# Kernel optimization log

Measured on AMD Instinct MI355X. Metric: run time of the kernel, lower is better.

Reference implementation:

```python
import jax, jax.numpy as jnp
import numpy as np

B, T, C, H = 2, 2048, 1024, 16
HD = C // H  # head dim = 64


def setup_inputs() -> dict:
    key = jax.random.key(0)
    k0, k1, k2 = jax.random.split(key, 3)
    x = jax.random.normal(k0, (B, T, C), jnp.float32)
    W_attn = jax.random.normal(k1, (C, 3 * C), jnp.float32) * 0.02
    b_attn = jnp.zeros((3 * C,), jnp.float32)
    W_proj = jax.random.normal(k2, (C, C), jnp.float32) * 0.02
    b_proj = jnp.zeros((C,), jnp.float32)
    # rope: (1,1,T,HD//2,2,2) stack of 2x2 rotation matrices [[cos,-sin],[sin,cos]]
    inv_freq = 1.0 / (10000.0 ** (jnp.arange(0, HD, 2, dtype=jnp.float32) / HD))
    ang = jnp.arange(T, dtype=jnp.float32)[:, None] * inv_freq[None, :]  # (T, HD//2)
    cos, sin = jnp.cos(ang), jnp.sin(ang)
    rope = jnp.stack([jnp.stack([cos, -sin], -1), jnp.stack([sin, cos], -1)], -2)
    rope = rope[None, None]  # (1,1,T,HD//2,2,2)
    return dict(x=x, W_attn=W_attn, b_attn=b_attn, W_proj=W_proj, b_proj=b_proj, rope=rope)


def reference(x, W_attn, b_attn, W_proj, b_proj, rope):
    Bv, Tv, Cv = x.shape
    Hd = Cv // H
    qkv = x @ W_attn + b_attn                      # (B,T,3C) fused QKV proj
    q, k, v = jnp.split(qkv, 3, axis=-1)

    def heads(t):
        return t.reshape(Bv, Tv, H, Hd).transpose(0, 2, 1, 3)  # (B,H,T,Hd)

    q, k, v = heads(q), heads(k), heads(v)

    cos = rope[..., 0, 0][..., None]               # (1,1,T,Hd//2,1)
    sin = rope[..., 1, 0][..., None]

    def rot(t):
        tr = t.reshape(Bv, H, Tv, Hd // 2, 2)
        xr, yr = tr[..., 0:1], tr[..., 1:2]
        out = jnp.concatenate([xr * cos - yr * sin, xr * sin + yr * cos], axis=-1)
        return out.reshape(Bv, H, Tv, Hd)

    q, k = rot(q), rot(k)

    scale = 1.0 / np.sqrt(Hd).astype(np.float32)
    att = jnp.einsum('bhqd,bhkd->bhqk', q, k) * scale
    mask = jnp.tril(jnp.ones((Tv, Tv), dtype=bool))  # causal
    att = jnp.where(mask[None, None], att, -jnp.inf)
    att = jax.nn.softmax(att, axis=-1)
    y = jnp.einsum('bhqk,bhkd->bhqd', att, v)
    y = y.transpose(0, 2, 1, 3).reshape(Bv, Tv, Cv)
    return y @ W_proj + b_proj
```

## Files before the change

kernel.cpp:

```cpp
#include <hip/hip_runtime.h>
#include <hip/hip_bf16.h>

typedef __attribute__((ext_vector_type(8))) short short8;
typedef __attribute__((ext_vector_type(4))) short short4b;
typedef __attribute__((ext_vector_type(4))) float f32x4;
typedef __attribute__((ext_vector_type(16))) float f32x16;
typedef __attribute__((ext_vector_type(4))) unsigned u32x4;

static constexpr int Bb = 2, Tt = 2048, Cc = 1024, Hh = 16;
static constexpr int BT = Bb * Tt;
static constexpr int N1 = 3 * Cc;
static constexpr float QS = 0.125f * 1.44269504f;

__device__ __forceinline__ unsigned short f2b(float f) {
  union { float f; unsigned u; } v; v.f = f;
  unsigned r = v.u + 0x7fffu + ((v.u >> 16) & 1u);
  return (unsigned short)(r >> 16);
}
__device__ __forceinline__ float b2f(short s) {
  union { unsigned u; float f; } v; v.u = ((unsigned)(unsigned short)s) << 16;
  return v.f;
}

__global__ __launch_bounds__(256) void k_cast(const float* __restrict__ in,
                                              unsigned short* __restrict__ out, int n) {
  int i = (blockIdx.x * 256 + threadIdx.x) * 8;
  if (i >= n) return;
  float4 a = *reinterpret_cast<const float4*>(in + i);
  float4 b = *reinterpret_cast<const float4*>(in + i + 4);
  short8 o;
  o[0] = f2b(a.x); o[1] = f2b(a.y); o[2] = f2b(a.z); o[3] = f2b(a.w);
  o[4] = f2b(b.x); o[5] = f2b(b.y); o[6] = f2b(b.z); o[7] = f2b(b.w);
  *reinterpret_cast<short8*>(out + i) = o;
}

__global__ __launch_bounds__(256) void k_tcast(const float* __restrict__ in,
                                               unsigned short* __restrict__ out,
                                               int R, int Ccol) {
  __shared__ float tile[32][33];
  int cb = blockIdx.x * 32, rb = blockIdx.y * 32;
  int tx = threadIdx.x & 31, ty = threadIdx.x >> 5;
  for (int i = 0; i < 32; i += 8)
    tile[ty + i][tx] = in[(size_t)(rb + ty + i) * Ccol + cb + tx];
  __syncthreads();
  for (int i = 0; i < 32; i += 8)
    out[(size_t)(cb + ty + i) * R + rb + tx] = f2b(tile[tx][ty + i]);
}

template <int BM, int NF, int EPI>
__global__ __launch_bounds__(512, 2)
void k_gemm8(const unsigned short* __restrict__ A, const unsigned short* __restrict__ Bt,
             const float* __restrict__ bias, void* __restrict__ Cout,
             const float* __restrict__ rope, unsigned short* __restrict__ Qs,
             unsigned short* __restrict__ Ks, unsigned short* __restrict__ Vt,
             int M, int N, int K) {
  constexpr int BN = NF * 64;
  constexpr int MF = BM / 32;
  constexpr int AI = BM / 64;
  constexpr int ASZ = BM * 64;
  constexpr int BSZ = BN * 64;
  constexpr int STRIDE = ASZ + BSZ;
  extern __shared__ unsigned short lds[];
  const int tid = threadIdx.x, lane = tid & 63, w = tid >> 6;
  const int wm = w >> 2, wn = w & 3;
  const int l15 = lane & 15, l4 = lane >> 4;
  int nbx = gridDim.x;
  int lin = blockIdx.y * nbx + blockIdx.x;
  int cpx = (nbx * gridDim.y) >> 3;
  lin = (lin & 7) * cpx + (lin >> 3);
  const int mb = lin / nbx, nb = lin % nbx;
  const size_t arow0 = (size_t)mb * BM;
  const size_t brow0 = (size_t)nb * BN;

  const int srow = lane >> 3;
  const int scol = (((lane & 7) * 16) ^ (srow << 4)) >> 1;
  auto stage = [&](int buf, int k0) {
    unsigned short* Ab = lds + buf * STRIDE;
    unsigned short* Bb = Ab + ASZ;
#pragma unroll
    for (int i = 0; i < AI; i++) {
      int c = w + 8 * i;
      const unsigned short* g = A + (arow0 + c * 8 + srow) * (size_t)K + k0 + scol;
      __builtin_amdgcn_global_load_lds((const __attribute__((address_space(1))) void*)g,
          (__attribute__((address_space(3))) void*)(Ab + c * 512), 16, 0, 0);
    }
#pragma unroll
    for (int i = 0; i < NF; i++) {
      int c = w + 8 * i;
      const unsigned short* g = Bt + (brow0 + c * 8 + srow) * (size_t)K + k0 + scol;
      __builtin_amdgcn_global_load_lds((const __attribute__((address_space(1))) void*)g,
          (__attribute__((address_space(3))) void*)(Bb + c * 512), 16, 0, 0);
    }
  };

  f32x4 acc[MF][NF] = {};
  const int NK = K >> 6;

  stage(0, 0);
  asm volatile("s_waitcnt vmcnt(0)" ::: "memory");
  asm volatile("s_barrier" ::: "memory");

  for (int kt = 0; kt < NK; kt++) {
    int buf = kt & 1;
    if (kt + 1 < NK) stage(buf ^ 1, (kt + 1) << 6);
    const unsigned short* Ab = lds + buf * STRIDE;
    const unsigned short* Bb = Ab + ASZ;
    short8 af[MF][2];
#pragma unroll
    for (int p = 0; p < NF; p++) {
      if (p == 0) {
#pragma unroll
        for (int m = 0; m < MF; m++) {
          int ra = wm * (BM / 2) + m * 16 + l15;
#pragma unroll
          for (int kk = 0; kk < 2; kk++) {
            int cb = (kk * 64 + l4 * 16) ^ ((ra & 7) << 4);
            af[m][kk] = *reinterpret_cast<const short8*>(Ab + ra * 64 + (cb >> 1));
          }
        }
      }
      short8 bfr[2];
      int rb = wn * (NF * 16) + p * 16 + l15;
#pragma unroll
      for (int kk = 0; kk < 2; kk++) {
        int cb = (kk * 64 + l4 * 16) ^ ((rb & 7) << 4);
        bfr[kk] = *reinterpret_cast<const short8*>(Bb + rb * 64 + (cb >> 1));
      }
      asm volatile("s_barrier" ::: "memory");
      asm volatile("s_waitcnt lgkmcnt(0)" ::: "memory");
      __builtin_amdgcn_sched_barrier(0);
      __builtin_amdgcn_s_setprio(1);
#pragma unroll
      for (int m = 0; m < MF; m++) {
        acc[m][p] = __builtin_amdgcn_mfma_f32_16x16x32_bf16(af[m][0], bfr[0], acc[m][p], 0, 0, 0);
        acc[m][p] = __builtin_amdgcn_mfma_f32_16x16x32_bf16(af[m][1], bfr[1], acc[m][p], 0, 0, 0);
      }
      __builtin_amdgcn_s_setprio(0);
      if (p == NF - 1)
        asm volatile("s_waitcnt vmcnt(0)" ::: "memory");
      asm volatile("s_barrier" ::: "memory");
    }
  }

#pragma unroll
  for (int m = 0; m < MF; m++) {
#pragma unroll
    for (int n = 0; n < NF; n++) {
      int ccol0 = nb * BN + wn * (NF * 16) + n * 16;
      float bv = bias[ccol0 + l15];
      int r0 = mb * BM + wm * (BM / 2) + m * 16 + l4 * 4;
      if (EPI == 0) {
#pragma unroll
        for (int j = 0; j < 4; j++)
          ((float*)Cout)[(size_t)(r0 + j) * N + ccol0 + l15] = acc[m][n][j] + bv;
      } else {
        int cls = ccol0 >> 10;
        int h = (ccol0 >> 6) & 15;
        int d = (ccol0 & 63) + l15;
        int bq = r0 >> 11;
        int t0 = r0 & 2047;
        size_t bh = (size_t)bq * 16 + h;
        if (cls == 2) {
          short4b o;
#pragma unroll
          for (int j = 0; j < 4; j++) o[j] = (short)f2b(acc[m][n][j] + bv);
          *reinterpret_cast<short4b*>(Vt + (bh * 64 + d) * Tt + t0) = o;
        } else {
          unsigned short* dst = (cls == 0) ? Qs : Ks;
          int jj = d >> 1;
          int odd = d & 1;
#pragma unroll
          for (int j = 0; j < 4; j++) {
            float v = acc[m][n][j] + bv;
            float part = __shfl_xor(v, 1);
            float2 sc = *reinterpret_cast<const float2*>(
                rope + (size_t)(t0 + j) * 128 + jj * 4 + 2);
            float x = odd ? part : v;
            float y = odd ? v : part;
            float rot = odd ? (x * sc.x + y * sc.y)
                            : (x * sc.y - y * sc.x);
            if (cls == 0) rot *= QS;
            dst[(bh * Tt + (t0 + j)) * 64 + d] = f2b(rot);
          }
        }
      }
    }
  }
}

__device__ __forceinline__ float tmax16(const f32x16& v) {
  float a0 = fmaxf(v[0], v[1]),   a1 = fmaxf(v[2], v[3]);
  float a2 = fmaxf(v[4], v[5]),   a3 = fmaxf(v[6], v[7]);
  float a4 = fmaxf(v[8], v[9]),   a5 = fmaxf(v[10], v[11]);
  float a6 = fmaxf(v[12], v[13]), a7 = fmaxf(v[14], v[15]);
  float b0 = fmaxf(a0, a1), b1 = fmaxf(a2, a3), b2 = fmaxf(a4, a5), b3 = fmaxf(a6, a7);
  return fmaxf(fmaxf(b0, b1), fmaxf(b2, b3));
}

template <int SLOT, bool DIAG>
__device__ __forceinline__ void tile64(
    const unsigned short* ldsp, const unsigned off_k[4], const unsigned off_v[4],
    int w, int l31, int hi, const short8 qf[4],
    float& m_run, float& l_run, f32x16 oacc[2], int grelBase) {
  constexpr int KB = SLOT * 8192;
  constexpr int VB = KB + 4096;
  f32x16 sc[2];
  const bool act0 = !DIAG || (grelBase <= w);
  const bool act1 = !DIAG || (grelBase + 1 <= w);
#pragma unroll
  for (int kt = 0; kt < 2; kt++) {
    if (DIAG && !(kt == 0 ? act0 : act1)) continue;
    f32x16 a = {};
    short8 kf[4];
#pragma unroll
    for (int kk = 0; kk < 4; kk++)
      kf[kk] = *reinterpret_cast<const short8*>(ldsp + KB + kt * 2048 + off_k[kk]);
    __builtin_amdgcn_s_setprio(1);
#pragma unroll
    for (int kk = 0; kk < 4; kk++)
      a = __builtin_amdgcn_mfma_f32_32x32x16_bf16(kf[kk], qf[kk], a, 0, 0, 0);
    __builtin_amdgcn_s_setprio(0);
    if (DIAG && grelBase + kt == w) {
#pragma unroll
      for (int r = 0; r < 16; r++) {
        int e = (r & 3) + 8 * (r >> 2) + 4 * hi;
        if (e > l31) a[r] = -1e30f;
      }
    }
    sc[kt] = a;
  }
  float km0 = act0 ? tmax16(sc[0]) : -1e30f;
  float km1 = act1 ? tmax16(sc[1]) : -1e30f;
  float mx = fmaxf(km0, km1);
  mx = fmaxf(mx, __shfl_xor(mx, 32));
  float fsc = 1.f;
  if (!__all(mx <= m_run + 8.f)) {
    float nm = fmaxf(m_run, mx);
    fsc = __builtin_amdgcn_exp2f(m_run - nm);
    m_run = nm;
#pragma unroll
    for (int dt = 0; dt < 2; dt++)
#pragma unroll
      for (int r = 0; r < 16; r++) oacc[dt][r] *= fsc;
  }
  l_run *= fsc;
#pragma unroll
  for (int kt = 0; kt < 2; kt++) {
    if (DIAG && !(kt == 0 ? act0 : act1)) continue;
    float p[16];
#pragma unroll
    for (int r = 0; r < 16; r++) p[r] = __builtin_amdgcn_exp2f(sc[kt][r] - m_run);
    float s0 = (p[0] + p[1]) + (p[2] + p[3]);
    float s1 = (p[4] + p[5]) + (p[6] + p[7]);
    float s2 = (p[8] + p[9]) + (p[10] + p[11]);
    float s3 = (p[12] + p[13]) + (p[14] + p[15]);
    l_run += (s0 + s1) + (s2 + s3);
    unsigned P[8];
#pragma unroll
    for (int i = 0; i < 8; i++)
      asm("v_cvt_pk_bf16_f32 %0, %1, %2" : "=v"(P[i]) : "v"(p[2 * i]), "v"(p[2 * i + 1]));
    unsigned Y0 = (unsigned)__shfl_xor((int)(hi ? P[0] : P[2]), 32);
    unsigned Y1 = (unsigned)__shfl_xor((int)(hi ? P[1] : P[3]), 32);
    unsigned Y2 = (unsigned)__shfl_xor((int)(hi ? P[4] : P[6]), 32);
    unsigned Y3 = (unsigned)__shfl_xor((int)(hi ? P[5] : P[7]), 32);
    u32x4 c0 = hi ? u32x4{Y0, Y1, P[2], P[3]} : u32x4{P[0], P[1], Y0, Y1};
    u32x4 c1 = hi ? u32x4{Y2, Y3, P[6], P[7]} : u32x4{P[4], P[5], Y2, Y3};
    short8 pf0 = __builtin_bit_cast(short8, c0);
    short8 pf1 = __builtin_bit_cast(short8, c1);
#pragma unroll
    for (int dt = 0; dt < 2; dt++) {
      short8 vf0 = *reinterpret_cast<const short8*>(ldsp + VB + dt * 2048 + off_v[kt * 2]);
      short8 vf1 = *reinterpret_cast<const short8*>(ldsp + VB + dt * 2048 + off_v[kt * 2 + 1]);
      __builtin_amdgcn_s_setprio(1);
      oacc[dt] = __builtin_amdgcn_mfma_f32_32x32x16_bf16(vf0, pf0, oacc[dt], 0, 0, 0);
      oacc[dt] = __builtin_amdgcn_mfma_f32_32x32x16_bf16(vf1, pf1, oacc[dt], 0, 0, 0);
      __builtin_amdgcn_s_setprio(0);
    }
  }
}

__global__ __launch_bounds__(256)
void k_attn1(const unsigned short* __restrict__ Qs, const unsigned short* __restrict__ Ks,
             const unsigned short* __restrict__ Vt, unsigned short* __restrict__ Opart,
             float* __restrict__ ml) {
  __shared__ unsigned short lds[16384];
  int tid = threadIdx.x, lane = tid & 63, w = tid >> 6;
  int sid = blockIdx.x;
  int qb = 15 - (sid >> 6);
  int c = (sid >> 5) & 1;
  int bh = sid & 31;
  int l31 = lane & 31, hi = lane >> 5;
  int qw0 = qb * 128 + w * 32;
  const unsigned short* Qb = Qs + (size_t)bh * Tt * 64;
  const unsigned short* Kb = Ks + (size_t)bh * Tt * 64;
  const unsigned short* Vb = Vt + (size_t)bh * 64 * Tt;

  short8 qf[4];
#pragma unroll
  for (int kk = 0; kk < 4; kk++)
    qf[kk] = *reinterpret_cast<const short8*>(Qb + (size_t)(qw0 + l31) * 64 + kk * 16 + hi * 8);

  const int sw = (l31 & 7) << 4;
  unsigned off_k[4], off_v[4];
#pragma unroll
  for (int kk = 0; kk < 4; kk++)
    off_k[kk] = (unsigned)(l31 * 128 + ((kk * 32 + hi * 16) ^ sw)) >> 1;
#pragma unroll
  for (int i = 0; i < 4; i++)
    off_v[i] = (unsigned)(l31 * 128 + (((i >> 1) * 64 + (i & 1) * 32 + hi * 16) ^ sw)) >> 1;

  const int r8 = lane >> 3;
  const int colb = ((lane & 7) * 16) ^ (r8 << 4);
  const unsigned short* gK0 = Kb + (size_t)(w * 8 + r8) * 64 + (colb >> 1);
  const unsigned short* gV0 = Vb + (size_t)(w * 8 + r8) * Tt + (colb >> 1);

  auto stage = [&](int slot, int T) {
    unsigned short* sb = lds + slot * 8192;
    const unsigned short* k0 = gK0 + (size_t)T * 4096;
    const unsigned short* v0 = gV0 + (size_t)T * 64;
    __builtin_amdgcn_global_load_lds((const __attribute__((address_space(1))) void*)k0,
        (__attribute__((address_space(3))) void*)(sb + w * 512), 16, 0, 0);
    __builtin_amdgcn_global_load_lds((const __attribute__((address_space(1))) void*)(k0 + 2048),
        (__attribute__((address_space(3))) void*)(sb + (w + 4) * 512), 16, 0, 0);
    __builtin_amdgcn_global_load_lds((const __attribute__((address_space(1))) void*)v0,
        (__attribute__((address_space(3))) void*)(sb + 4096 + w * 512), 16, 0, 0);
    __builtin_amdgcn_global_load_lds((const __attribute__((address_space(1))) void*)(v0 + (size_t)32 * Tt),
        (__attribute__((address_space(3))) void*)(sb + 4096 + (w + 4) * 512), 16, 0, 0);
  };

  const int NT = 2 * qb + 2, half = NT >> 1;
  const int t0 = c ? half : 0, t1 = c ? NT : half;
  const int diagT = 2 * qb;

  float m_run = -1e30f, l_run = 0.f;
  f32x16 oacc[2] = {};

  stage(0, t0);
  if (t0 + 1 < t1) {
    stage(1, t0 + 1);
    asm volatile("s_waitcnt vmcnt(4)" ::: "memory");
  } else {
    asm volatile("s_waitcnt vmcnt(0)" ::: "memory");
  }
  asm volatile("s_barrier" ::: "memory");

  int sl = 0;
  for (int T = t0; T < t1; ++T) {
    int gB = 2 * T - 4 * qb;
    bool full = T < diagT;
    if (sl == 0) {
      if (full) tile64<0, false>(lds, off_k, off_v, w, l31, hi, qf, m_run, l_run, oacc, 0);
      else      tile64<0, true >(lds, off_k, off_v, w, l31, hi, qf, m_run, l_run, oacc, gB);
    } else {
      if (full) tile64<1, false>(lds, off_k, off_v, w, l31, hi, qf, m_run, l_run, oacc, 0);
      else      tile64<1, true >(lds, off_k, off_v, w, l31, hi, qf, m_run, l_run, oacc, gB);
    }
    if (T + 1 < t1) {
      asm volatile("s_barrier" ::: "memory");
      if (T + 2 < t1) {
        stage(sl, T + 2);
        asm volatile("s_waitcnt vmcnt(4)" ::: "memory");
      } else {
        asm volatile("s_waitcnt vmcnt(0)" ::: "memory");
      }
      asm volatile("s_barrier" ::: "memory");
    }
    sl ^= 1;
  }

  l_run += __shfl_xor(l_run, 32);

  size_t orow = (size_t)sid * 128 + w * 32 + l31;
#pragma unroll
  for (int dt = 0; dt < 2; dt++)
#pragma unroll
    for (int q4 = 0; q4 < 4; q4++) {
      short4b oo;
#pragma unroll
      for (int jj = 0; jj < 4; jj++) oo[jj] = (short)f2b(oacc[dt][q4 * 4 + jj]);
      *reinterpret_cast<short4b*>(Opart + orow * 64 + dt * 32 + q4 * 8 + hi * 4) = oo;
    }
  if (hi == 0) {
    float2 v; v.x = m_run; v.y = l_run;
    *reinterpret_cast<float2*>(ml + orow * 2) = v;
  }
}

__global__ __launch_bounds__(256)
void k_attn2(const unsigned short* __restrict__ Opart, const float* __restrict__ ml,
             unsigned short* __restrict__ Y) {
  int gid = blockIdx.x * 256 + threadIdx.x;
  int row = gid >> 3;
  int dblk = (gid & 7) * 8;
  int bh = row >> 11, q = row & 2047;
  int qb = q >> 7, qrow = q & 127;
  int s0 = (15 - qb) * 64 + bh;
  int s1 = s0 + 32;
  float2 ml0 = *reinterpret_cast<const float2*>(ml + ((size_t)s0 * 128 + qrow) * 2);
  float2 ml1 = *reinterpret_cast<const float2*>(ml + ((size_t)s1 * 128 + qrow) * 2);
  float m = fmaxf(ml0.x, ml1.x);
  float w0 = __builtin_amdgcn_exp2f(ml0.x - m);
  float w1 = __builtin_amdgcn_exp2f(ml1.x - m);
  float inv = 1.0f / (w0 * ml0.y + w1 * ml1.y);
  float a0 = w0 * inv, a1 = w1 * inv;
  short8 o0 = *reinterpret_cast<const short8*>(Opart + ((size_t)s0 * 128 + qrow) * 64 + dblk);
  short8 o1 = *reinterpret_cast<const short8*>(Opart + ((size_t)s1 * 128 + qrow) * 64 + dblk);
  short8 o;
#pragma unroll
  for (int j = 0; j < 8; j++) o[j] = (short)f2b(b2f(o0[j]) * a0 + b2f(o1[j]) * a1);
  int b = bh >> 4, h = bh & 15;
  *reinterpret_cast<short8*>(Y + ((size_t)(b * Tt + q)) * Cc + h * 64 + dblk) = o;
}

extern "C" void kernel_launch(void* const* d_in, const int* in_sizes, int n_in,
                              void* d_out, int out_size, void* d_ws, size_t ws_size,
                              hipStream_t stream) {
  (void)in_sizes; (void)n_in; (void)out_size; (void)ws_size;
  const float* x      = (const float*)d_in[0];
  const float* W_attn = (const float*)d_in[1];
  const float* b_attn = (const float*)d_in[2];
  const float* W_proj = (const float*)d_in[3];
  const float* b_proj = (const float*)d_in[4];
  const float* rope   = (const float*)d_in[5];
  float* out = (float*)d_out;

  char* ws = (char*)d_ws;
  unsigned short* xb    = (unsigned short*)(ws);
  unsigned short* WaT   = (unsigned short*)(ws + (8u << 20));
  unsigned short* WpT   = (unsigned short*)(ws + (14u << 20));
  unsigned short* Qs    = (unsigned short*)(ws + (16u << 20));
  unsigned short* Ks    = (unsigned short*)(ws + (24u << 20));
  unsigned short* Vt    = (unsigned short*)(ws + (32u << 20));
  unsigned short* Yb    = (unsigned short*)(ws + (40u << 20));
  unsigned short* Opart = (unsigned short*)(ws + (48u << 20));
  float*          ml    = (float*)(ws + (64u << 20));

  constexpr int LDS_QKV  = (128 + 192) * 64 * 2 * 2;
  constexpr int LDS_PROJ = (128 + 128) * 64 * 2 * 2;
  (void)hipFuncSetAttribute(reinterpret_cast<const void*>(&k_gemm8<128, 3, 1>),
                            hipFuncAttributeMaxDynamicSharedMemorySize, LDS_QKV);
  (void)hipFuncSetAttribute(reinterpret_cast<const void*>(&k_gemm8<128, 2, 0>),
                            hipFuncAttributeMaxDynamicSharedMemorySize, LDS_PROJ);

  k_cast<<<2048, 256, 0, stream>>>(x, xb, BT * Cc);
  k_tcast<<<dim3(N1 / 32, Cc / 32), 256, 0, stream>>>(W_attn, WaT, Cc, N1);
  k_tcast<<<dim3(Cc / 32, Cc / 32), 256, 0, stream>>>(W_proj, WpT, Cc, Cc);
  k_gemm8<128, 3, 1><<<dim3(N1 / 192, BT / 128), 512, LDS_QKV, stream>>>(
      xb, WaT, b_attn, nullptr, rope, Qs, Ks, Vt, BT, N1, Cc);
  k_attn1<<<1024, 256, 0, stream>>>(Qs, Ks, Vt, Opart, ml);
  k_attn2<<<2048, 256, 0, stream>>>(Opart, ml, Yb);
  k_gemm8<128, 2, 0><<<dim3(Cc / 128, BT / 128), 512, LDS_PROJ, stream>>>(
      Yb, WpT, b_proj, out, nullptr, nullptr, nullptr, nullptr, BT, Cc, Cc);
}
```

Baseline: 109.5 us.

## Reorder attention block schedule and simplify K/V staging pipeline

Block IDs in the split-KV attention kernel are remapped so the first two rounds (c=0, c=1) cover query blocks from heaviest to lightest and the last two rounds cover them lightest to heaviest. This is meant to balance per-CU work across the causal triangle. The K/V prefetch now stages only the next tile at the top of each iteration and uses plain __syncthreads, replacing the two-ahead staging with manual vmcnt waits and barriers, so there is less prefetch depth than before. The combine kernel's indexing is updated to match the new block layout.

```diff
diff --git a/kernel.cpp b/kernel.cpp
--- a/kernel.cpp
+++ b/kernel.cpp
@@ -286,9 +286,12 @@
   __shared__ unsigned short lds[16384];
   int tid = threadIdx.x, lane = tid & 63, w = tid >> 6;
   int sid = blockIdx.x;
-  int qb = 15 - (sid >> 6);
-  int c = (sid >> 5) & 1;
-  int bh = sid & 31;
+  int r = sid >> 8;
+  int p = sid & 255;
+  int j = p >> 5;
+  int bh = p & 31;
+  int qb = (r < 2) ? (15 - j) : j;
+  int c = r & 1;
   int l31 = lane & 31, hi = lane >> 5;
   int qw0 = qb * 128 + w * 32;
   const unsigned short* Qb = Qs + (size_t)bh * Tt * 64;
@@ -336,16 +339,10 @@
   f32x16 oacc[2] = {};
 
   stage(0, t0);
-  if (t0 + 1 < t1) {
-    stage(1, t0 + 1);
-    asm volatile("s_waitcnt vmcnt(4)" ::: "memory");
-  } else {
-    asm volatile("s_waitcnt vmcnt(0)" ::: "memory");
-  }
-  asm volatile("s_barrier" ::: "memory");
-
+  __syncthreads();
   int sl = 0;
   for (int T = t0; T < t1; ++T) {
+    if (T + 1 < t1) stage(sl ^ 1, T + 1);
     int gB = 2 * T - 4 * qb;
     bool full = T < diagT;
     if (sl == 0) {
@@ -355,16 +352,7 @@
       if (full) tile64<1, false>(lds, off_k, off_v, w, l31, hi, qf, m_run, l_run, oacc, 0);
       else      tile64<1, true >(lds, off_k, off_v, w, l31, hi, qf, m_run, l_run, oacc, gB);
     }
-    if (T + 1 < t1) {
-      asm volatile("s_barrier" ::: "memory");
-      if (T + 2 < t1) {
-        stage(sl, T + 2);
-        asm volatile("s_waitcnt vmcnt(4)" ::: "memory");
-      } else {
-        asm volatile("s_waitcnt vmcnt(0)" ::: "memory");
-      }
-      asm volatile("s_barrier" ::: "memory");
-    }
+    __syncthreads();
     sl ^= 1;
   }
 
@@ -394,8 +382,8 @@
   int dblk = (gid & 7) * 8;
   int bh = row >> 11, q = row & 2047;
   int qb = q >> 7, qrow = q & 127;
-  int s0 = (15 - qb) * 64 + bh;
-  int s1 = s0 + 32;
+  int s0 = (qb >= 8) ? ((15 - qb) * 32 + bh) : (512 + qb * 32 + bh);
+  int s1 = s0 + 256;
   float2 ml0 = *reinterpret_cast<const float2*>(ml + ((size_t)s0 * 128 + qrow) * 2);
   float2 ml1 = *reinterpret_cast<const float2*>(ml + ((size_t)s1 * 128 + qrow) * 2);
   float m = fmaxf(ml0.x, ml1.x);
@@ -407,7 +395,7 @@
   short8 o1 = *reinterpret_cast<const short8*>(Opart + ((size_t)s1 * 128 + qrow) * 64 + dblk);
   short8 o;
 #pragma unroll
-  for (int j = 0; j < 8; j++) o[j] = (short)f2b(b2f(o0[j]) * a0 + b2f(o1[j]) * a1);
+  for (int jj = 0; jj < 8; jj++) o[jj] = (short)f2b(b2f(o0[jj]) * a0 + b2f(o1[jj]) * a1);
   int b = bh >> 4, h = bh & 15;
   *reinterpret_cast<short8*>(Y + ((size_t)(b * Tt + q)) * Cc + h * 64 + dblk) = o;
 }
```

Result: slower. 114.6 us (+4.7%).
